# Kernel optimization log

Measured on AMD Instinct MI355X. Metric: run time of the kernel, lower is better.

Reference implementation:

```python
import jax, jax.numpy as jnp
import numpy as np

N_HEAD = 16
D_MODEL = 1024
HEAD_SIZE = D_MODEL // N_HEAD
BATCH, SEQ = 2, 2048


def setup_inputs() -> dict:
    key = jax.random.key(0)
    ks = jax.random.split(key, 11)
    s = 1.0 / np.sqrt(D_MODEL)
    inp = {
        "query": jax.random.normal(ks[0], (BATCH, SEQ, D_MODEL), jnp.float32),
        "key_in": jax.random.normal(ks[1], (BATCH, SEQ, D_MODEL), jnp.float32),
        "value": jax.random.normal(ks[2], (BATCH, SEQ, D_MODEL), jnp.float32),
        # per-head Q/K/V projections stacked: [n_head, d_model, head_size]
        "Wq": jax.random.uniform(ks[3], (N_HEAD, D_MODEL, HEAD_SIZE), jnp.float32, -s, s),
        "Wk": jax.random.uniform(ks[4], (N_HEAD, D_MODEL, HEAD_SIZE), jnp.float32, -s, s),
        "Wv": jax.random.uniform(ks[5], (N_HEAD, D_MODEL, HEAD_SIZE), jnp.float32, -s, s),
        "bq": jax.random.uniform(ks[6], (N_HEAD, HEAD_SIZE), jnp.float32, -s, s),
        "bk": jax.random.uniform(ks[7], (N_HEAD, HEAD_SIZE), jnp.float32, -s, s),
        "bv": jax.random.uniform(ks[8], (N_HEAD, HEAD_SIZE), jnp.float32, -s, s),
        "Wo": jax.random.uniform(ks[9], (D_MODEL, D_MODEL), jnp.float32, -s, s),
        "bo": jax.random.uniform(ks[10], (D_MODEL,), jnp.float32, -s, s),
    }
    return inp


def reference(query, key_in, value, Wq, Wk, Wv, bq, bk, bv, Wo, bo):
    # Per-head projections fused into one einsum each: [b, h, s, k]
    Q = jnp.einsum("bsd,hdk->bhsk", query, Wq) + bq[:, None, :]
    K = jnp.einsum("bsd,hdk->bhsk", key_in, Wk) + bk[:, None, :]
    V = jnp.einsum("bsd,hdk->bhsk", value, Wv) + bv[:, None, :]
    scale = 1.0 / np.sqrt(HEAD_SIZE)
    wei = jnp.einsum("bhqk,bhsk->bhqs", Q, K) * scale  # [b, h, s, s]
    wei = jax.nn.softmax(wei, axis=-1)
    out = jnp.einsum("bhqs,bhsk->bhqk", wei, V)  # [b, h, s, k]
    b, h, s, k = out.shape
    out = out.transpose(0, 2, 1, 3).reshape(b, s, h * k)
    return out @ Wo.T + bo
```

## Files before the change

kernel.cpp:

```cpp
#include <hip/hip_runtime.h>
#include <hip/hip_bf16.h>

typedef __attribute__((ext_vector_type(8))) short short8;
typedef __attribute__((ext_vector_type(4))) short bf16x4;
typedef __attribute__((ext_vector_type(4))) float f32x4;

#define DM 1024
#define NH 16
#define HS 64
#define SEQL 2048

__device__ __forceinline__ float bf2f(short s) {
  unsigned u = ((unsigned)(unsigned short)s) << 16;
  float f;
  __builtin_memcpy(&f, &u, 4);
  return f;
}
__device__ __forceinline__ short f2bf(float f) {
  unsigned u;
  __builtin_memcpy(&u, &f, 4);
  u = u + 0x7FFFu + ((u >> 16) & 1u);
  return (short)(u >> 16);
}

__device__ __forceinline__ void gl2lds16(const void* g, void* l) {
  __builtin_amdgcn_global_load_lds(
      (const __attribute__((address_space(1))) void*)g,
      (__attribute__((address_space(3))) void*)l, 16, 0, 0);
}

__device__ __forceinline__ short8 cvt_pk8(f32x4 lo, f32x4 hi) {
  union { short8 s8; unsigned u[4]; } r;
  asm("v_cvt_pk_bf16_f32 %0, %1, %2" : "=v"(r.u[0]) : "v"(lo[0]), "v"(lo[1]));
  asm("v_cvt_pk_bf16_f32 %0, %1, %2" : "=v"(r.u[1]) : "v"(lo[2]), "v"(lo[3]));
  asm("v_cvt_pk_bf16_f32 %0, %1, %2" : "=v"(r.u[2]) : "v"(hi[0]), "v"(hi[1]));
  asm("v_cvt_pk_bf16_f32 %0, %1, %2" : "=v"(r.u[3]) : "v"(hi[2]), "v"(hi[3]));
  return r.s8;
}

__global__ __launch_bounds__(256) void pack_w_kernel(
    const float* __restrict__ Wq, const float* __restrict__ Wk, const float* __restrict__ Wv,
    short* __restrict__ WtQ, short* __restrict__ WtK, short* __restrict__ WtV) {
  const float* W = (blockIdx.z == 0) ? Wq : (blockIdx.z == 1) ? Wk : Wv;
  short* Wt      = (blockIdx.z == 0) ? WtQ : (blockIdx.z == 1) ? WtK : WtV;
  __shared__ short Ts[64][73];
  const int h = blockIdx.y, dm0 = blockIdx.x * 64;
  const int tid = threadIdx.x;
#pragma unroll
  for (int p = 0; p < 4; ++p) {
    int idx = p * 256 + tid;
    int i = idx >> 4, hsq = (idx & 15) * 4;
    f32x4 v = *(const f32x4*)&W[((h << 10) + dm0 + i) * 64 + hsq];
#pragma unroll
    for (int j = 0; j < 4; ++j) Ts[i][hsq + j] = f2bf(v[j]);
  }
  __syncthreads();
  {
    int hs = tid >> 2, dmq = (tid & 3) * 16;
    short8 o0, o1;
#pragma unroll
    for (int j = 0; j < 8; ++j) { o0[j] = Ts[dmq + j][hs]; o1[j] = Ts[dmq + 8 + j][hs]; }
    short* dst = &Wt[((h * 64 + hs) << 10) + dm0 + dmq];
    *(short8*)dst = o0;
    *(short8*)(dst + 8) = o1;
  }
}

__global__ __launch_bounds__(256) void cvt_bf16_kernel(const float* __restrict__ in,
                                                       short* __restrict__ out) {
  int i = blockIdx.x * 256 + threadIdx.x;
  const f32x4* p = (const f32x4*)(in + (size_t)i * 8);
  f32x4 a = p[0], b = p[1];
  short8 o;
#pragma unroll
  for (int j = 0; j < 4; ++j) { o[j] = f2bf(a[j]); o[4 + j] = f2bf(b[j]); }
  *(short8*)(out + (size_t)i * 8) = o;
}

struct GemmArgs {
  const void* A;
  const void* Bt;
  const float* bias;
  short* out;
  float* outf;
  int mode;
};

template <bool AF32, int NB>
__global__ __launch_bounds__(256) void gemm_bt_kernel(GemmArgs g0, GemmArgs g1, GemmArgs g2) {
  GemmArgs g = (blockIdx.z == 0) ? g0 : (blockIdx.z == 1) ? g1 : g2;
  const int K = 1024;
  const int TN = NB * 32;
  const int m0 = blockIdx.x * 128;
  const int n0 = blockIdx.y * TN;
  const int tid = threadIdx.x;
  const int w = tid >> 6, l = tid & 63, lr = l & 15, lk = l >> 4;
  const int wr = w >> 1, wc = w & 1;

  __shared__ __align__(16) char AsRaw[2][128 * 32 * (AF32 ? 4 : 2)];
  __shared__ __align__(16) short Bs[2][TN * 32];

  const int swz3 = lr & 7;
  const int swz2 = (lr & 3) ^ ((lr >> 2) & 3);

  f32x4 acc[4][NB];
#pragma unroll
  for (int i = 0; i < 4; ++i)
#pragma unroll
    for (int j = 0; j < NB; ++j) acc[i][j] = (f32x4){0.f, 0.f, 0.f, 0.f};

  auto STAGE = [&](int buf, int k0) {
    if constexpr (AF32) {
      const float* Af = (const float*)g.A;
      float* Asf = (float*)AsRaw[buf];
#pragma unroll
      for (int i = 0; i < 4; ++i) {
        int c = i * 256 + tid;
        int row = c >> 3, s = c & 7;
        int gc = (s ^ (row & 7)) * 4;
        gl2lds16(&Af[(size_t)(m0 + row) * K + k0 + gc], &Asf[c * 4]);
      }
    } else {
      const short* Ah = (const short*)g.A;
      short* As = (short*)AsRaw[buf];
#pragma unroll
      for (int i = 0; i < 2; ++i) {
        int c = i * 256 + tid;
        int row = c >> 2, s = c & 3;
        int gc = (s ^ ((row & 3) ^ ((row >> 2) & 3))) * 8;
        gl2lds16(&Ah[(size_t)(m0 + row) * K + k0 + gc], &As[c * 8]);
      }
    }
    const short* Bh = (const short*)g.Bt;
#pragma unroll
    for (int i = 0; i < TN / 64; ++i) {
      int c = i * 256 + tid;
      int row = c >> 2, s = c & 3;
      int gc = (s ^ ((row & 3) ^ ((row >> 2) & 3))) * 8;
      gl2lds16(&Bh[(size_t)(n0 + row) * K + k0 + gc], &Bs[buf][c * 8]);
    }
  };

  auto COMPUTE = [&](int buf) {
    const float* Asf = (const float*)AsRaw[buf];
    const short* As  = (const short*)AsRaw[buf];
    short8 af[4], bfr[NB];
#pragma unroll
    for (int t = 0; t < 4; ++t) {
      int row = wr * 64 + t * 16 + lr;
      if constexpr (AF32) {
        int base = row * 32;
        f32x4 lo = *(const f32x4*)&Asf[base + (((lk << 1)    ) ^ swz3) * 4];
        f32x4 hi = *(const f32x4*)&Asf[base + (((lk << 1) | 1) ^ swz3) * 4];
        af[t] = cvt_pk8(lo, hi);
      } else {
        af[t] = *(const short8*)&As[row * 32 + (lk ^ swz2) * 8];
      }
    }
#pragma unroll
    for (int t = 0; t < NB; ++t) {
      int row = wc * (NB * 16) + t * 16 + lr;
      bfr[t] = *(const short8*)&Bs[buf][row * 32 + (lk ^ swz2) * 8];
    }
#pragma unroll
    for (int ti = 0; ti < 4; ++ti)
#pragma unroll
      for (int tj = 0; tj < NB; ++tj)
        acc[ti][tj] = __builtin_amdgcn_mfma_f32_16x16x32_bf16(af[ti], bfr[tj], acc[ti][tj], 0, 0, 0);
  };

  STAGE(0, 0);
  __syncthreads();
  int cur = 0;
  for (int t = 0; t < 31; ++t) {
    STAGE(cur ^ 1, (t + 1) * 32);
    COMPUTE(cur);
    __syncthreads();
    cur ^= 1;
  }
  COMPUTE(cur);

#pragma unroll
  for (int ti = 0; ti < 4; ++ti)
#pragma unroll
    for (int tj = 0; tj < NB; ++tj) {
      int n = n0 + wc * (NB * 16) + tj * 16 + lr;
      float bia = g.bias[n];
      int mb = m0 + wr * 64 + ti * 16 + lk * 4;
      if (g.mode == 2) {
        bf16x4 o;
#pragma unroll
        for (int r = 0; r < 4; ++r) o[r] = f2bf(acc[ti][tj][r] + bia);
        *(bf16x4*)&g.out[((mb >> 11) * 16 + (n >> 6)) * (SEQL * HS) + (n & 63) * SEQL + (mb & 2047)] = o;
      } else {
#pragma unroll
        for (int r = 0; r < 4; ++r) {
          int m = mb + r;
          float v = acc[ti][tj][r] + bia;
          if (g.mode == 0) {
            g.out[((m >> 11) * 16 + (n >> 6)) * (SEQL * HS) + (m & 2047) * HS + (n & 63)] = f2bf(v);
          } else {
            g.outf[(size_t)m * DM + n] = v;
          }
        }
      }
    }
}

__global__ __launch_bounds__(256, 3) void attn_kernel(const short* __restrict__ Qg, const short* __restrict__ Kg,
                                                      const short* __restrict__ Vtg, short* __restrict__ Og) {
  const int qt = blockIdx.x;
  const int bh = blockIdx.y;
  const short* Qp = Qg + bh * SEQL * HS;
  const short* Kp = Kg + bh * SEQL * HS;
  const short* Vp = Vtg + bh * HS * SEQL;
  const int tid = threadIdx.x, w = tid >> 6, l = tid & 63, lr = l & 15, lk = l >> 4;
  const int qw = qt * 64 + w * 16;

  __shared__ __align__(16) short Ks[128][72];
  __shared__ __align__(16) short Vt[64][136];

  short8 qf[2];
#pragma unroll
  for (int kk = 0; kk < 2; ++kk) {
    short8 qr = *(const short8*)&Qp[(qw + lr) * HS + kk * 32 + lk * 8];
#pragma unroll
    for (int j = 0; j < 8; ++j) qf[kk][j] = f2bf(bf2f(qr[j]) * 0.125f);
  }

  float mrow = -1e30f, lrow = 0.f;
  f32x4 accO[4];
#pragma unroll
  for (int t = 0; t < 4; ++t) accO[t] = (f32x4){0.f, 0.f, 0.f, 0.f};

  short8 kreg[4], vreg[4];
  auto loadKV = [&](int kv) {
#pragma unroll
    for (int i = 0; i < 4; ++i) {
      int q = tid + i * 256;
      kreg[i] = *(const short8*)&Kp[(kv * 128 + (q >> 3)) * HS + (q & 7) * 8];
      vreg[i] = *(const short8*)&Vp[(q >> 4) * SEQL + kv * 128 + (q & 15) * 8];
    }
  };
  loadKV(0);

  for (int kv = 0; kv < 16; ++kv) {
    __syncthreads();
#pragma unroll
    for (int i = 0; i < 4; ++i) {
      int q = tid + i * 256;
      *(short8*)&Ks[q >> 3][(q & 7) * 8] = kreg[i];
      *(short8*)&Vt[q >> 4][(q & 15) * 8] = vreg[i];
    }
    __syncthreads();
    if (kv < 15) loadKV(kv + 1);

    f32x4 accS[8];
#pragma unroll
    for (int tj = 0; tj < 8; ++tj) {
      short8 a0 = *(const short8*)&Ks[tj * 16 + lr][lk * 8];
      short8 a1 = *(const short8*)&Ks[tj * 16 + lr][32 + lk * 8];
      f32x4 z = (f32x4){0.f, 0.f, 0.f, 0.f};
      z = __builtin_amdgcn_mfma_f32_16x16x32_bf16(a0, qf[0], z, 0, 0, 0);
      accS[tj] = __builtin_amdgcn_mfma_f32_16x16x32_bf16(a1, qf[1], z, 0, 0, 0);
    }

    float mx = accS[0][0];
#pragma unroll
    for (int tj = 0; tj < 8; ++tj)
#pragma unroll
      for (int r = 0; r < 4; ++r) mx = fmaxf(mx, accS[tj][r]);
    mx = fmaxf(mx, __shfl_xor(mx, 16));
    mx = fmaxf(mx, __shfl_xor(mx, 32));
    float mn = fmaxf(mrow, mx);
    float alpha = __expf(mrow - mn);
    float ps = 0.f;
#pragma unroll
    for (int tj = 0; tj < 8; ++tj)
#pragma unroll
      for (int r = 0; r < 4; ++r) {
        float p = __expf(accS[tj][r] - mn);
        accS[tj][r] = p;
        ps += p;
      }
    ps += __shfl_xor(ps, 16);
    ps += __shfl_xor(ps, 32);
    lrow = lrow * alpha + ps;
    mrow = mn;
#pragma unroll
    for (int t = 0; t < 4; ++t) accO[t] *= alpha;

#pragma unroll
    for (int st = 0; st < 8; ++st) {
      bf16x4 bfrag;
#pragma unroll
      for (int r = 0; r < 4; ++r) bfrag[r] = f2bf(accS[st][r]);
#pragma unroll
      for (int tjd = 0; tjd < 4; ++tjd) {
        bf16x4 afrag = *(const bf16x4*)&Vt[tjd * 16 + lr][st * 16 + lk * 4];
        accO[tjd] = __builtin_amdgcn_mfma_f32_16x16x16bf16_1k(afrag, bfrag, accO[tjd], 0, 0, 0);
      }
    }
  }

  const int b = bh >> 4, h = bh & 15;
  float inv = 1.f / lrow;
  size_t rowbase = (size_t)(b * SEQL + qw + lr) * DM + h * HS;
#pragma unroll
  for (int tjd = 0; tjd < 4; ++tjd) {
    bf16x4 o;
#pragma unroll
    for (int r = 0; r < 4; ++r) o[r] = f2bf(accO[tjd][r] * inv);
    *(bf16x4*)&Og[rowbase + tjd * 16 + lk * 4] = o;
  }
}

extern "C" void kernel_launch(void* const* d_in, const int* in_sizes, int n_in,
                              void* d_out, int out_size, void* d_ws, size_t ws_size,
                              hipStream_t stream) {
  const float* query  = (const float*)d_in[0];
  const float* key_in = (const float*)d_in[1];
  const float* value  = (const float*)d_in[2];
  const float* Wq = (const float*)d_in[3];
  const float* Wk = (const float*)d_in[4];
  const float* Wv = (const float*)d_in[5];
  const float* bq = (const float*)d_in[6];
  const float* bk = (const float*)d_in[7];
  const float* bv = (const float*)d_in[8];
  const float* Wo = (const float*)d_in[9];
  const float* bo = (const float*)d_in[10];
  float* out = (float*)d_out;

  short* ws  = (short*)d_ws;
  short* Qb  = ws;
  short* Kb  = Qb + (4 << 20);
  short* Vbt = Kb + (4 << 20);
  short* X   = Vbt + (4 << 20);
  short* WtQ = X;
  short* WtK = WtQ + (1 << 20);
  short* WtV = WtK + (1 << 20);
  short* At  = X;
  short* Wob = Qb;

  pack_w_kernel<<<dim3(16, 16, 3), 256, 0, stream>>>(Wq, Wk, Wv, WtQ, WtK, WtV);

  GemmArgs gq{query, WtQ, bq, Qb, nullptr, 0}, gk{key_in, WtK, bk, Kb, nullptr, 0},
           gv{value, WtV, bv, Vbt, nullptr, 2};
  gemm_bt_kernel<true, 4><<<dim3(32, 8, 3), 256, 0, stream>>>(gq, gk, gv);

  attn_kernel<<<dim3(32, 32), 256, 0, stream>>>(Qb, Kb, Vbt, At);

  cvt_bf16_kernel<<<dim3(512), 256, 0, stream>>>(Wo, Wob);

  GemmArgs go{At, Wob, bo, nullptr, out, 1};
  gemm_bt_kernel<false, 2><<<dim3(32, 16, 1), 256, 0, stream>>>(go, go, go);
}
```

Baseline: 259.7 us.

## Fold softmax scale and log2e into Q projection, use exp2 with lazy rescale

Q is now scaled by 0.125*log2(e) in the QKV projection epilogue, so the attention kernel loads Q directly and computes exp2 instead of exp. The online softmax skips rescaling the accumulator unless the row max grows by more than 8 (in log2 units). The change also adds packed bf16 conversion for the P fragments and raises wave priority around the MFMA loops. Together these cut per-iteration VALU work in the attention inner loop. The threshold-based lazy rescale lets unnormalized values grow up to about 2^8, which slightly changes numerics.

```diff
diff --git a/kernel.cpp b/kernel.cpp
--- a/kernel.cpp
+++ b/kernel.cpp
@@ -9,6 +9,7 @@
 #define NH 16
 #define HS 64
 #define SEQL 2048
+#define QSCALE 0.18033688011112042f
 
 __device__ __forceinline__ float bf2f(short s) {
   unsigned u = ((unsigned)(unsigned short)s) << 16;
@@ -36,6 +37,12 @@
   asm("v_cvt_pk_bf16_f32 %0, %1, %2" : "=v"(r.u[2]) : "v"(hi[0]), "v"(hi[1]));
   asm("v_cvt_pk_bf16_f32 %0, %1, %2" : "=v"(r.u[3]) : "v"(hi[2]), "v"(hi[3]));
   return r.s8;
+}
+__device__ __forceinline__ bf16x4 cvt_pk4(f32x4 v) {
+  union { bf16x4 s4; unsigned u[2]; } r;
+  asm("v_cvt_pk_bf16_f32 %0, %1, %2" : "=v"(r.u[0]) : "v"(v[0]), "v"(v[1]));
+  asm("v_cvt_pk_bf16_f32 %0, %1, %2" : "=v"(r.u[1]) : "v"(v[2]), "v"(v[3]));
+  return r.s4;
 }
 
 __global__ __launch_bounds__(256) void pack_w_kernel(
@@ -84,6 +91,7 @@
   short* out;
   float* outf;
   int mode;
+  float oscale;
 };
 
 template <bool AF32, int NB>
@@ -198,7 +206,7 @@
           int m = mb + r;
           float v = acc[ti][tj][r] + bia;
           if (g.mode == 0) {
-            g.out[((m >> 11) * 16 + (n >> 6)) * (SEQL * HS) + (m & 2047) * HS + (n & 63)] = f2bf(v);
+            g.out[((m >> 11) * 16 + (n >> 6)) * (SEQL * HS) + (m & 2047) * HS + (n & 63)] = f2bf(v * g.oscale);
           } else {
             g.outf[(size_t)m * DM + n] = v;
           }
@@ -222,11 +230,8 @@
 
   short8 qf[2];
 #pragma unroll
-  for (int kk = 0; kk < 2; ++kk) {
-    short8 qr = *(const short8*)&Qp[(qw + lr) * HS + kk * 32 + lk * 8];
-#pragma unroll
-    for (int j = 0; j < 8; ++j) qf[kk][j] = f2bf(bf2f(qr[j]) * 0.125f);
-  }
+  for (int kk = 0; kk < 2; ++kk)
+    qf[kk] = *(const short8*)&Qp[(qw + lr) * HS + kk * 32 + lk * 8];
 
   float mrow = -1e30f, lrow = 0.f;
   f32x4 accO[4];
@@ -256,6 +261,7 @@
     if (kv < 15) loadKV(kv + 1);
 
     f32x4 accS[8];
+    __builtin_amdgcn_s_setprio(1);
 #pragma unroll
     for (int tj = 0; tj < 8; ++tj) {
       short8 a0 = *(const short8*)&Ks[tj * 16 + lr][lk * 8];
@@ -264,6 +270,7 @@
       z = __builtin_amdgcn_mfma_f32_16x16x32_bf16(a0, qf[0], z, 0, 0, 0);
       accS[tj] = __builtin_amdgcn_mfma_f32_16x16x32_bf16(a1, qf[1], z, 0, 0, 0);
     }
+    __builtin_amdgcn_s_setprio(0);
 
     float mx = accS[0][0];
 #pragma unroll
@@ -272,35 +279,38 @@
       for (int r = 0; r < 4; ++r) mx = fmaxf(mx, accS[tj][r]);
     mx = fmaxf(mx, __shfl_xor(mx, 16));
     mx = fmaxf(mx, __shfl_xor(mx, 32));
-    float mn = fmaxf(mrow, mx);
-    float alpha = __expf(mrow - mn);
+    if (__any(mx - mrow > 8.f)) {
+      float mn = fmaxf(mrow, mx);
+      float al = exp2f(mrow - mn);
+      lrow *= al;
+#pragma unroll
+      for (int t = 0; t < 4; ++t) accO[t] *= al;
+      mrow = mn;
+    }
     float ps = 0.f;
 #pragma unroll
     for (int tj = 0; tj < 8; ++tj)
 #pragma unroll
       for (int r = 0; r < 4; ++r) {
-        float p = __expf(accS[tj][r] - mn);
+        float p = exp2f(accS[tj][r] - mrow);
         accS[tj][r] = p;
         ps += p;
       }
     ps += __shfl_xor(ps, 16);
     ps += __shfl_xor(ps, 32);
-    lrow = lrow * alpha + ps;
-    mrow = mn;
-#pragma unroll
-    for (int t = 0; t < 4; ++t) accO[t] *= alpha;
-
+    lrow += ps;
+
+    __builtin_amdgcn_s_setprio(1);
 #pragma unroll
     for (int st = 0; st < 8; ++st) {
-      bf16x4 bfrag;
-#pragma unroll
-      for (int r = 0; r < 4; ++r) bfrag[r] = f2bf(accS[st][r]);
+      bf16x4 bfrag = cvt_pk4(accS[st]);
 #pragma unroll
       for (int tjd = 0; tjd < 4; ++tjd) {
         bf16x4 afrag = *(const bf16x4*)&Vt[tjd * 16 + lr][st * 16 + lk * 4];
         accO[tjd] = __builtin_amdgcn_mfma_f32_16x16x16bf16_1k(afrag, bfrag, accO[tjd], 0, 0, 0);
       }
     }
+    __builtin_amdgcn_s_setprio(0);
   }
 
   const int b = bh >> 4, h = bh & 15;
@@ -344,14 +354,15 @@
 
   pack_w_kernel<<<dim3(16, 16, 3), 256, 0, stream>>>(Wq, Wk, Wv, WtQ, WtK, WtV);
 
-  GemmArgs gq{query, WtQ, bq, Qb, nullptr, 0}, gk{key_in, WtK, bk, Kb, nullptr, 0},
-           gv{value, WtV, bv, Vbt, nullptr, 2};
+  GemmArgs gq{query, WtQ, bq, Qb, nullptr, 0, QSCALE},
+           gk{key_in, WtK, bk, Kb, nullptr, 0, 1.0f},
+           gv{value, WtV, bv, Vbt, nullptr, 2, 1.0f};
   gemm_bt_kernel<true, 4><<<dim3(32, 8, 3), 256, 0, stream>>>(gq, gk, gv);
 
   attn_kernel<<<dim3(32, 32), 256, 0, stream>>>(Qb, Kb, Vbt, At);
 
   cvt_bf16_kernel<<<dim3(512), 256, 0, stream>>>(Wo, Wob);
 
-  GemmArgs go{At, Wob, bo, nullptr, out, 1};
+  GemmArgs go{At, Wob, bo, nullptr, out, 1, 1.0f};
   gemm_bt_kernel<false, 2><<<dim3(32, 16, 1), 256, 0, stream>>>(go, go, go);
 }
```

Result: slower. 274.1 us (+5.6%).
